# Performance work log

Measured on AMD Instinct MI355X. Metric: run time of the kernel, lower is better.

## Reference

```python
import jax, jax.numpy as jnp
import numpy as np

EPS = 1e-6
LN_EPS = 1e-6

def _mlstm_parallel_stabilized(q, k, v, igate_preact, fgate_preact):
    # q,k,v: (B,NH,S,DH); igate_preact,fgate_preact: (B,NH,S,1)
    B, NH, S, DH = q.shape
    log_fg = jax.nn.log_sigmoid(fgate_preact[..., 0])            # (B,NH,S)
    cs = jnp.cumsum(log_fg, axis=-1)                             # (B,NH,S)
    # log decay matrix: entry (i,j) = cumsum_i - cumsum_j, lower-triangular (j<=i)
    fg_mat = cs[..., :, None] - cs[..., None, :]                 # (B,NH,S,S)
    mask = jnp.tril(jnp.ones((S, S), dtype=bool))
    log_D = jnp.where(mask, fg_mat + igate_preact[..., 0][..., None, :], -jnp.inf)
    max_log_D = jnp.max(log_D, axis=-1, keepdims=True)           # (B,NH,S,1)
    D = jnp.exp(log_D - max_log_D)                               # (B,NH,S,S)
    k_scaled = k / jnp.sqrt(jnp.float32(DH)).astype(k.dtype)
    qk = jnp.einsum('bhsd,bhtd->bhst', q, k_scaled)              # (B,NH,S,S)
    C = qk * D
    normalizer = jnp.maximum(jnp.abs(jnp.sum(C, axis=-1, keepdims=True)), jnp.exp(-max_log_D))
    C_norm = C / (normalizer + EPS)
    return jnp.einsum('bhst,bhtd->bhsd', C_norm, v)              # (B,NH,S,DH)

def _multihead_layernorm(x, weight):
    # x: (B,NH,S,DH), weight: (NH,DH); normalize over DH per head, no bias
    mu = jnp.mean(x, axis=-1, keepdims=True)
    var = jnp.mean(jnp.square(x - mu), axis=-1, keepdims=True)
    xn = (x - mu) * jax.lax.rsqrt(var + LN_EPS)
    return xn * weight[None, :, None, :]

def setup_inputs() -> dict:
    key = jax.random.key(0)
    ks = jax.random.split(key, 6)
    B, S, E, NH = 2, 2048, 1024, 8
    q = jax.random.normal(ks[0], (B, S, E), dtype=jnp.float32)
    k = jax.random.normal(ks[1], (B, S, E), dtype=jnp.float32)
    v = jax.random.normal(ks[2], (B, S, E), dtype=jnp.float32)
    igate_kernel = jnp.zeros((3 * E, NH), dtype=jnp.float32)
    igate_bias = 0.1 * jax.random.normal(ks[3], (NH,), dtype=jnp.float32)
    fgate_kernel = jnp.zeros((3 * E, NH), dtype=jnp.float32)
    fgate_bias = jnp.linspace(3.0, 6.0, NH, dtype=jnp.float32)
    outnorm_weight = jnp.ones((NH, E // NH), dtype=jnp.float32)
    return {"q": q, "k": k, "v": v,
            "igate_kernel": igate_kernel, "igate_bias": igate_bias,
            "fgate_kernel": fgate_kernel, "fgate_bias": fgate_bias,
            "outnorm_weight": outnorm_weight}

def reference(q, k, v, igate_kernel, igate_bias, fgate_kernel, fgate_bias, outnorm_weight):
    B, S, E = q.shape
    NH = igate_bias.shape[0]
    qkv = jnp.concatenate([q, k, v], axis=-1)                    # (B,S,3E)
    igate_preact = qkv @ igate_kernel + igate_bias               # (B,S,NH)
    fgate_preact = qkv @ fgate_kernel + fgate_bias               # (B,S,NH)
    qh = q.reshape(B, S, NH, -1).transpose(0, 2, 1, 3)           # (B,NH,S,DH)
    kh = k.reshape(B, S, NH, -1).transpose(0, 2, 1, 3)
    vh = v.reshape(B, S, NH, -1).transpose(0, 2, 1, 3)
    ig = igate_preact.transpose(0, 2, 1)[..., None]              # (B,NH,S,1)
    fg = fgate_preact.transpose(0, 2, 1)[..., None]
    h = _mlstm_parallel_stabilized(qh, kh, vh, ig, fg)           # (B,NH,S,DH)
    h_norm = _multihead_layernorm(h, outnorm_weight)
    return h_norm.transpose(0, 2, 1, 3).reshape(B, S, -1)        # (B,S,E)
```

## Files before the change

### kernel.cpp

```cpp
#include <hip/hip_runtime.h>
#include <math.h>

#define S_LEN 2048
#define E_DIM 1024
#define NHEAD 8
#define DHEAD 128

typedef short bf16x8 __attribute__((ext_vector_type(8)));
typedef float f32x4 __attribute__((ext_vector_type(4)));
typedef unsigned int u32x4 __attribute__((ext_vector_type(4)));
typedef unsigned int u32x2 __attribute__((ext_vector_type(2)));

constexpr float RSQ_DH  = 0.08838834764831843f;
constexpr float LNRSQ   = -2.4260151319598084f;
constexpr float EPS_NORM = 1e-6f;
constexpr float LN_EPS_C = 1e-6f;

__device__ inline unsigned bfpair(float lo, float hi) {
  unsigned a = __builtin_bit_cast(unsigned, lo);
  unsigned b = __builtin_bit_cast(unsigned, hi);
  a = (a + 0x7fffu + ((a >> 16) & 1u)) >> 16;
  b = (b + 0x7fffu + ((b >> 16) & 1u)) >> 16;
  return a | (b << 16);
}

__device__ inline unsigned cvtpk(float lo, float hi) {
  unsigned r;
  asm("v_cvt_pk_bf16_f32 %0, %1, %2" : "=v"(r) : "v"(lo), "v"(hi));
  return r;
}

__device__ inline void gload_lds16(const void* g, void* lds) {
  __builtin_amdgcn_global_load_lds(
      (const __attribute__((address_space(1))) unsigned int*)g,
      (__attribute__((address_space(3))) unsigned int*)lds, 16, 0, 0);
}
__device__ inline void gload_lds4(const void* g, void* lds) {
  __builtin_amdgcn_global_load_lds(
      (const __attribute__((address_space(1))) unsigned int*)g,
      (__attribute__((address_space(3))) unsigned int*)lds, 4, 0, 0);
}

__global__ __launch_bounds__(256) void gates_fused(
    const float* __restrict__ q, const float* __restrict__ k, const float* __restrict__ v,
    const float* __restrict__ Wi, const float* __restrict__ bi,
    const float* __restrict__ Wf, const float* __restrict__ bf,
    float* __restrict__ ig_pre, float* __restrict__ fg_pre,
    unsigned short* __restrict__ kb) {
  const int t = threadIdx.x;
  const int row0 = blockIdx.x * 4;
  const int b = row0 >> 11;
  const int s0 = row0 & 2047;
  float p[4][16];
#pragma unroll
  for (int rr = 0; rr < 4; ++rr)
#pragma unroll
    for (int c = 0; c < 16; ++c) p[rr][c] = 0.f;

#pragma unroll
  for (int i = 0; i < 3; ++i) {
    const float* base = (i == 0) ? q : (i == 1) ? k : v;
    float xs[4][4];
#pragma unroll
    for (int rr = 0; rr < 4; ++rr) {
      const float4 xv = *(const float4*)(base + (size_t)(row0 + rr) * E_DIM + t * 4);
      xs[rr][0] = xv.x; xs[rr][1] = xv.y; xs[rr][2] = xv.z; xs[rr][3] = xv.w;
    }
#pragma unroll
    for (int j = 0; j < 4; ++j) {
      const int ge = i * E_DIM + t * 4 + j;
      const float4 wiA = *(const float4*)(Wi + (size_t)ge * 8);
      const float4 wiB = *(const float4*)(Wi + (size_t)ge * 8 + 4);
      const float4 wfA = *(const float4*)(Wf + (size_t)ge * 8);
      const float4 wfB = *(const float4*)(Wf + (size_t)ge * 8 + 4);
      const float wv16[16] = {wiA.x, wiA.y, wiA.z, wiA.w, wiB.x, wiB.y, wiB.z, wiB.w,
                              wfA.x, wfA.y, wfA.z, wfA.w, wfB.x, wfB.y, wfB.z, wfB.w};
#pragma unroll
      for (int rr = 0; rr < 4; ++rr) {
        const float x = xs[rr][j];
#pragma unroll
        for (int c = 0; c < 16; ++c) p[rr][c] += x * wv16[c];
      }
    }
    if (i == 1 && kb != nullptr) {
      const int h = (t * 4) >> 7, d = (t * 4) & 127;
#pragma unroll
      for (int rr = 0; rr < 4; ++rr) {
        u32x2 pk;
        pk.x = bfpair(xs[rr][0], xs[rr][1]);
        pk.y = bfpair(xs[rr][2], xs[rr][3]);
        *(u32x2*)(kb + (((size_t)b * NHEAD + h) * S_LEN + (s0 + rr)) * DHEAD + d) = pk;
      }
    }
  }

#pragma unroll
  for (int rr = 0; rr < 4; ++rr)
#pragma unroll
    for (int c = 0; c < 16; ++c) {
      float val = p[rr][c];
      val += __shfl_xor(val, 1);
      val += __shfl_xor(val, 2);
      val += __shfl_xor(val, 4);
      val += __shfl_xor(val, 8);
      val += __shfl_xor(val, 16);
      val += __shfl_xor(val, 32);
      p[rr][c] = val;
    }
  __shared__ float sred[4][4][16];
  const int wid = t >> 6, lane = t & 63;
  if (lane == 0) {
#pragma unroll
    for (int rr = 0; rr < 4; ++rr)
#pragma unroll
      for (int c = 0; c < 16; ++c) sred[wid][rr][c] = p[rr][c];
  }
  __syncthreads();
  if (t < 64) {
    const int rr = t >> 4, c = t & 15;
    float sum = sred[0][rr][c] + sred[1][rr][c] + sred[2][rr][c] + sred[3][rr][c];
    const int h = c & 7;
    const int row = row0 + rr;
    const int bb = row / S_LEN, s = row % S_LEN;
    if (c < 8) ig_pre[((size_t)bb * NHEAD + h) * S_LEN + s] = sum + bi[h];
    else       fg_pre[((size_t)bb * NHEAD + h) * S_LEN + s] = sum + bf[h];
  }
}

__global__ __launch_bounds__(256) void vtrans(const float* __restrict__ v,
                                              unsigned short* __restrict__ vtb) {
  __shared__ unsigned int tile[128][36];
  const int bid = blockIdx.x;
  const int bh = bid >> 5, st = bid & 31;
  const int b = bh >> 3, h = bh & 7;
  const int s0 = st * 64;
  const int t = threadIdx.x;
#pragma unroll
  for (int i = 0; i < 4; ++i) {
    const int task = t + 256 * i;
    const int sp = task & 31, dq = task >> 5;
    const float* src = v + ((size_t)b * S_LEN + s0 + 2 * sp) * E_DIM + h * DHEAD + dq * 4;
    const float4 r0 = *(const float4*)(src);
    const float4 r1 = *(const float4*)(src + E_DIM);
    tile[dq * 4 + 0][sp] = bfpair(r0.x, r1.x);
    tile[dq * 4 + 1][sp] = bfpair(r0.y, r1.y);
    tile[dq * 4 + 2][sp] = bfpair(r0.z, r1.z);
    tile[dq * 4 + 3][sp] = bfpair(r0.w, r1.w);
  }
  __syncthreads();
#pragma unroll
  for (int i = 0; i < 2; ++i) {
    const int task = t + 256 * i;
    const int d = task >> 2, c4 = task & 3;
    u32x4 w0, w1;
    w0.x = tile[d][c4 * 8 + 0]; w0.y = tile[d][c4 * 8 + 1];
    w0.z = tile[d][c4 * 8 + 2]; w0.w = tile[d][c4 * 8 + 3];
    w1.x = tile[d][c4 * 8 + 4]; w1.y = tile[d][c4 * 8 + 5];
    w1.z = tile[d][c4 * 8 + 6]; w1.w = tile[d][c4 * 8 + 7];
    unsigned short* dst = vtb + ((size_t)bh * DHEAD + d) * S_LEN + s0 + c4 * 16;
    *(u32x4*)(dst)     = w0;
    *(u32x4*)(dst + 8) = w1;
  }
}

__global__ __launch_bounds__(256) void scan_kernel(
    const float* __restrict__ ig_pre, const float* __restrict__ fg_pre,
    float* __restrict__ cs_out, float* __restrict__ g_out, float* __restrict__ gmax_out,
    float g_add) {
  const int bhh = blockIdx.x;
  const int t = threadIdx.x;
  const int lane = t & 63, wid = t >> 6;
  const size_t base = (size_t)bhh * S_LEN;
  float vals[8];
  float run = 0.f;
#pragma unroll
  for (int i = 0; i < 8; ++i) {
    const float x = fg_pre[base + t * 8 + i];
    const float lf = fminf(x, 0.f) - log1pf(__expf(-fabsf(x)));
    run += lf;
    vals[i] = run;
  }
  float ws = run;
#pragma unroll
  for (int off = 1; off < 64; off <<= 1) {
    const float v = __shfl_up(ws, off);
    if (lane >= off) ws += v;
  }
  __shared__ float wsum[4];
  if (lane == 63) wsum[wid] = ws;
  __syncthreads();
  float wpre = 0.f;
#pragma unroll
  for (int kk = 0; kk < 4; ++kk)
    if (kk < wid) wpre += wsum[kk];
  const float prefix = wpre + (ws - run);

  float g_loc[8], gm_loc[8];
  float lmax = -3.4e38f;
#pragma unroll
  for (int i = 0; i < 8; ++i) {
    const float csv = vals[i] + prefix;
    vals[i] = csv;
    const float gg = ig_pre[base + t * 8 + i] - csv;
    g_loc[i] = gg;
    lmax = fmaxf(lmax, gg);
    gm_loc[i] = lmax;
  }
  float wm = lmax;
#pragma unroll
  for (int off = 1; off < 64; off <<= 1) {
    const float v = __shfl_up(wm, off);
    if (lane >= off) wm = fmaxf(wm, v);
  }
  __shared__ float wmax[4];
  if (lane == 63) wmax[wid] = wm;
  __syncthreads();
  float mpre = -3.4e38f;
#pragma unroll
  for (int kk = 0; kk < 4; ++kk)
    if (kk < wid) mpre = fmaxf(mpre, wmax[kk]);
  float excl = __shfl_up(wm, 1);
  if (lane == 0) excl = -3.4e38f;
  const float pmax = fmaxf(mpre, excl);

#pragma unroll
  for (int i = 0; i < 8; ++i) {
    cs_out[base + t * 8 + i]   = vals[i];
    g_out[base + t * 8 + i]    = g_loc[i] + g_add;
    gmax_out[base + t * 8 + i] = fmaxf(gm_loc[i], pmax);
  }
}

__global__ __launch_bounds__(256) void mlstm_mfma9(
    const unsigned short* __restrict__ kb, const unsigned short* __restrict__ vtb,
    const float* __restrict__ q,
    const float* __restrict__ cs, const float* __restrict__ garr, const float* __restrict__ gmax,
    const float* __restrict__ wgt, float* __restrict__ out) {
  __shared__ __align__(16) unsigned char kbuf[4][8192];
  __shared__ __align__(16) unsigned char vbuf[4][8192];
  __shared__ float g_sh[4][32];
  __shared__ float den_sh[4][64];

  const int bid = blockIdx.x;
  int qb;
  if (bid < 256) qb = 31 - (bid >> 4);
  else           qb = (bid - 256) >> 4;
  const int g16 = bid & 15;
  const int bh = 2 * (g16 & 7) + (g16 >> 3);
  const int b = bh >> 3, h = bh & 7;
  const int t = threadIdx.x;
  const int w = t >> 6;
  const int iw = w & 1;
  const int tp = w >> 1;
  const int l = t & 63;
  const int r = l & 15;
  const int qq = l >> 4;
  const size_t bhS = (size_t)bh * S_LEN;

  const int grA = qb * 64 + 4 * r + 2 * iw;
  const int grB = grA + 1;
  const float gmA = gmax[bhS + grA];
  const float gmB = gmax[bhS + grB];
  const float rAB = __expf(gmA - gmB);

  bf16x8 qfA[4], qfB[4];
  {
    const float* qrowA = q + ((size_t)b * S_LEN + grA) * E_DIM + h * DHEAD;
    const float* qrowB = q + ((size_t)b * S_LEN + grB) * E_DIM + h * DHEAD;
#pragma unroll
    for (int c = 0; c < 4; ++c) {
      float4 f0 = *(const float4*)(qrowA + 32 * c + 8 * qq);
      float4 f1 = *(const float4*)(qrowA + 32 * c + 8 * qq + 4);
      u32x4 u;
      u.x = bfpair(f0.x, f0.y); u.y = bfpair(f0.z, f0.w);
      u.z = bfpair(f1.x, f1.y); u.w = bfpair(f1.z, f1.w);
      qfA[c] = __builtin_bit_cast(bf16x8, u);
      f0 = *(const float4*)(qrowB + 32 * c + 8 * qq);
      f1 = *(const float4*)(qrowB + 32 * c + 8 * qq + 4);
      u.x = bfpair(f0.x, f0.y); u.y = bfpair(f0.z, f0.w);
      u.z = bfpair(f1.x, f1.y); u.w = bfpair(f1.z, f1.w);
      qfB[c] = __builtin_bit_cast(bf16x8, u);
    }
  }

  f32x4 oA[8], oB[8];
#pragma unroll
  for (int n = 0; n < 8; ++n) { oA[n] = (f32x4){0,0,0,0}; oB[n] = (f32x4){0,0,0,0}; }
  float denA = 0.f, denB = 0.f;

  const unsigned short* kt = kb + bhS * DHEAD;
  const unsigned short* vt = vtb + (size_t)bh * DHEAD * S_LEN;

  auto stage = [&](int pair, int set) {
    const int j0 = pair * 64 + tp * 32;
    const int bi = set * 2 + tp;
#pragma unroll
    for (int a = 0; a < 4; ++a) {
      const int m = iw * 256 + a * 64 + l;
      const int u = m ^ ((m >> 4) & 7);
      gload_lds16(kt + ((size_t)(j0 + (u >> 4))) * DHEAD + (u & 15) * 8,
                  &kbuf[bi][(iw * 256 + a * 64) * 16]);
    }
#pragma unroll
    for (int a = 0; a < 4; ++a) {
      const int m = iw * 256 + a * 64 + l;
      const int u = m ^ ((m >> 3) & 7);
      gload_lds16(vt + (size_t)(u >> 2) * S_LEN + j0 + (u & 3) * 8,
                  &vbuf[bi][(iw * 256 + a * 64) * 16]);
    }
    if (l < 32) gload_lds4(garr + bhS + j0 + l, &g_sh[bi][0]);
  };

  auto body = [&](int j0, int bi, bool diag) {
    __builtin_amdgcn_s_setprio(1);
    f32x4 sA0 = {0,0,0,0}, sA1 = {0,0,0,0}, sB0 = {0,0,0,0}, sB1 = {0,0,0,0};
#pragma unroll
    for (int c = 0; c < 4; ++c) {
      const int u0 = ((r)      * 16 + 4 * c + qq) ^ (r & 7);
      const int u1 = ((16 + r) * 16 + 4 * c + qq) ^ (r & 7);
      bf16x8 ka0 = *(const bf16x8*)&kbuf[bi][u0 * 16];
      bf16x8 ka1 = *(const bf16x8*)&kbuf[bi][u1 * 16];
      sA0 = __builtin_amdgcn_mfma_f32_16x16x32_bf16(ka0, qfA[c], sA0, 0, 0, 0);
      sB0 = __builtin_amdgcn_mfma_f32_16x16x32_bf16(ka0, qfB[c], sB0, 0, 0, 0);
      sA1 = __builtin_amdgcn_mfma_f32_16x16x32_bf16(ka1, qfA[c], sA1, 0, 0, 0);
      sB1 = __builtin_amdgcn_mfma_f32_16x16x32_bf16(ka1, qfB[c], sB1, 0, 0, 0);
    }
    __builtin_amdgcn_s_setprio(0);

    unsigned PA0[2], PA1[2], PB0[2], PB1[2];
    {
      float wa[4], wb[4];
#pragma unroll
      for (int m = 0; m < 4; ++m) {
        const int jl = 4 * qq + m;
        const float e = __expf(g_sh[bi][jl] - gmA);
        float a = sA0[m] * e;
        float bq = sB0[m] * e * rAB;
        if (diag) {
          if (j0 + jl > grA) a = 0.f;
          if (j0 + jl > grB) bq = 0.f;
        }
        wa[m] = a; wb[m] = bq; denA += a; denB += bq;
      }
      PA0[0] = cvtpk(wa[0], wa[1]); PA0[1] = cvtpk(wa[2], wa[3]);
      PB0[0] = cvtpk(wb[0], wb[1]); PB0[1] = cvtpk(wb[2], wb[3]);
#pragma unroll
      for (int m = 0; m < 4; ++m) {
        const int jl = 16 + 4 * qq + m;
        const float e = __expf(g_sh[bi][jl] - gmA);
        float a = sA1[m] * e;
        float bq = sB1[m] * e * rAB;
        if (diag) {
          if (j0 + jl > grA) a = 0.f;
          if (j0 + jl > grB) bq = 0.f;
        }
        wa[m] = a; wb[m] = bq; denA += a; denB += bq;
      }
      PA1[0] = cvtpk(wa[0], wa[1]); PA1[1] = cvtpk(wa[2], wa[3]);
      PB1[0] = cvtpk(wb[0], wb[1]); PB1[1] = cvtpk(wb[2], wb[3]);
    }

    unsigned AA[4], AB[4];
#pragma unroll
    for (int m = 0; m < 4; ++m) {
      const int srcl = r + 16 * (2 * (qq & 1) + (m >> 1));
      const unsigned a0 = (unsigned)__shfl((int)PA0[m & 1], srcl);
      const unsigned a1 = (unsigned)__shfl((int)PA1[m & 1], srcl);
      const unsigned b0 = (unsigned)__shfl((int)PB0[m & 1], srcl);
      const unsigned b1 = (unsigned)__shfl((int)PB1[m & 1], srcl);
      AA[m] = (qq < 2) ? a0 : a1;
      AB[m] = (qq < 2) ? b0 : b1;
    }
    u32x4 ua, ub;
    ua.x = AA[0]; ua.y = AA[1]; ua.z = AA[2]; ua.w = AA[3];
    ub.x = AB[0]; ub.y = AB[1]; ub.z = AB[2]; ub.w = AB[3];
    const bf16x8 paA = __builtin_bit_cast(bf16x8, ua);
    const bf16x8 paB = __builtin_bit_cast(bf16x8, ub);

    __builtin_amdgcn_s_setprio(1);
#pragma unroll
    for (int n = 0; n < 8; ++n) {
      const int ud = (16 * n + r) * 4 + qq;
      const int up = ud ^ ((ud >> 3) & 7);
      bf16x8 vb = *(const bf16x8*)&vbuf[bi][up * 16];
      oA[n] = __builtin_amdgcn_mfma_f32_16x16x32_bf16(paA, vb, oA[n], 0, 0, 0);
      oB[n] = __builtin_amdgcn_mfma_f32_16x16x32_bf16(paB, vb, oB[n], 0, 0, 0);
    }
    __builtin_amdgcn_s_setprio(0);
  };

  stage(0, 0);
  for (int p = 0; p < qb; ++p) {
    stage(p + 1, (p + 1) & 1);
    asm volatile("s_waitcnt vmcnt(9)" ::: "memory");
    __builtin_amdgcn_sched_barrier(0);
    __syncthreads();
    body(p * 64 + tp * 32, (p & 1) * 2 + tp, false);
    __syncthreads();
  }
  asm volatile("s_waitcnt vmcnt(0)" ::: "memory");
  __builtin_amdgcn_sched_barrier(0);
  __syncthreads();
  body(qb * 64 + tp * 32, (qb & 1) * 2 + tp, true);

  float* osh = (float*)&kbuf[0][0];
  __syncthreads();
  const int xsw = (r & 7) << 2;
  if (tp == 1) {
#pragma unroll
    for (int n = 0; n < 8; ++n) {
      const int i0 = ((((16 * n + r) * 2 + iw) * 2 + 0) * 16 + 4 * qq) ^ xsw;
      const int i1 = ((((16 * n + r) * 2 + iw) * 2 + 1) * 16 + 4 * qq) ^ xsw;
      *(f32x4*)&osh[i0] = oA[n];
      *(f32x4*)&osh[i1] = oB[n];
    }
    den_sh[iw * 2 + 0][l] = denA;
    den_sh[iw * 2 + 1][l] = denB;
  }
  __syncthreads();
  if (tp == 0) {
    denA += den_sh[iw * 2 + 0][l];
    denB += den_sh[iw * 2 + 1][l];
#pragma unroll
    for (int n = 0; n < 8; ++n) {
      const int i0 = ((((16 * n + r) * 2 + iw) * 2 + 0) * 16 + 4 * qq) ^ xsw;
      const int i1 = ((((16 * n + r) * 2 + iw) * 2 + 1) * 16 + 4 * qq) ^ xsw;
      oA[n] += *(const f32x4*)&osh[i0];
      oB[n] += *(const f32x4*)&osh[i1];
    }

    const float* wrow = wgt + h * DHEAD;
    float wv_n[8];
#pragma unroll
    for (int n = 0; n < 8; ++n) wv_n[n] = wrow[16 * n + r];

#pragma unroll
    for (int fg = 0; fg < 2; ++fg) {
      float den_f = (fg == 0) ? denA : denB;
      den_f += __shfl_xor(den_f, 16);
      den_f += __shfl_xor(den_f, 32);
#pragma unroll
      for (int m = 0; m < 4; ++m) {
        const int iloc = 4 * qq + m;
        const float den_o = __shfl(den_f, iloc);
        const int grow = qb * 64 + 4 * iloc + 2 * iw + fg;
        const float csg = cs[bhS + grow];
        const float gmg = gmax[bhS + grow];
        const float norm = fmaxf(fabsf(den_o), __expf(-(csg + gmg))) + EPS_NORM;
        const float inv = 1.f / norm;
        float hv[8];
        float s1 = 0.f, s2 = 0.f;
#pragma unroll
        for (int n = 0; n < 8; ++n) {
          hv[n] = ((fg == 0) ? oA[n][m] : oB[n][m]) * inv;
          s1 += hv[n]; s2 += hv[n] * hv[n];
        }
        s1 += __shfl_xor(s1, 1); s1 += __shfl_xor(s1, 2);
        s1 += __shfl_xor(s1, 4); s1 += __shfl_xor(s1, 8);
        s2 += __shfl_xor(s2, 1); s2 += __shfl_xor(s2, 2);
        s2 += __shfl_xor(s2, 4); s2 += __shfl_xor(s2, 8);
        const float mu  = s1 * (1.f / 128.f);
        const float var = s2 * (1.f / 128.f) - mu * mu;
        const float rstd = rsqrtf(var + LN_EPS_C);
        float* orow = out + ((size_t)b * S_LEN + grow) * E_DIM + h * DHEAD;
#pragma unroll
        for (int n = 0; n < 8; ++n)
          orow[16 * n + r] = (hv[n] - mu) * rstd * wv_n[n];
      }
    }
  }
}

__global__ __launch_bounds__(256) void mlstm_mfma(
    const float* __restrict__ q, const float* __restrict__ k, const float* __restrict__ v,
    const float* __restrict__ cs, const float* __restrict__ garr, const float* __restrict__ gmax,
    const float* __restrict__ wgt, float* __restrict__ out) {
  __shared__ unsigned short k_lds[32][136];
  __shared__ unsigned int   vt_u32[128][20];
  __shared__ unsigned int   xch[4][16][20];
  __shared__ float          g_sh[32];

  const int bid = blockIdx.x;
  int qt;
  if (bid < 256) qt = 31 - (bid >> 4);
  else           qt = (bid - 256) >> 4;
  const int bh = bid & 15;
  const int b = bh >> 3, h = bh & 7;
  const int t = threadIdx.x;
  const int w = t >> 6;
  const int l = t & 63;
  const int r = l & 15;
  const int qq = l >> 4;
  const size_t bhS = (size_t)bh * S_LEN;

  const int gr = qt * 64 + 4 * r + w;
  const float gm_lane = gmax[bhS + gr];

  bf16x8 qfrag[4];
  {
    const float* qrow = q + ((size_t)b * S_LEN + gr) * E_DIM + h * DHEAD;
#pragma unroll
    for (int c = 0; c < 4; ++c) {
      const float4 f0 = *(const float4*)(qrow + 32 * c + 8 * qq);
      const float4 f1 = *(const float4*)(qrow + 32 * c + 8 * qq + 4);
      u32x4 u;
      u.x = bfpair(f0.x, f0.y); u.y = bfpair(f0.z, f0.w);
      u.z = bfpair(f1.x, f1.y); u.w = bfpair(f1.z, f1.w);
      qfrag[c] = __builtin_bit_cast(bf16x8, u);
    }
  }

  f32x4 o[8];
#pragma unroll
  for (int n = 0; n < 8; ++n) o[n] = (f32x4){0.f, 0.f, 0.f, 0.f};
  float den_p = 0.f;

  const int kj = t >> 3, ks = t & 7;
  const int vjp = t & 15, vds = t >> 4;

  const int ntiles = 2 * qt + 2;
  for (int jt = 0; jt < ntiles; ++jt) {
    const int j0 = jt * 32;
    {
      const float* src = k + ((size_t)b * S_LEN + j0 + kj) * E_DIM + h * DHEAD + ks * 16;
      float4 f0 = *(const float4*)(src);
      float4 f1 = *(const float4*)(src + 4);
      float4 f2 = *(const float4*)(src + 8);
      float4 f3 = *(const float4*)(src + 12);
      u32x4 ua, ub;
      ua.x = bfpair(f0.x, f0.y); ua.y = bfpair(f0.z, f0.w);
      ua.z = bfpair(f1.x, f1.y); ua.w = bfpair(f1.z, f1.w);
      ub.x = bfpair(f2.x, f2.y); ub.y = bfpair(f2.z, f2.w);
      ub.z = bfpair(f3.x, f3.y); ub.w = bfpair(f3.z, f3.w);
      *(u32x4*)&k_lds[kj][ks * 16]     = ua;
      *(u32x4*)&k_lds[kj][ks * 16 + 8] = ub;
    }
    {
      const float* s0 = v + ((size_t)b * S_LEN + j0 + 2 * vjp) * E_DIM + h * DHEAD + vds * 8;
      const float* s1 = s0 + E_DIM;
      float4 a0 = *(const float4*)(s0);
      float4 a1 = *(const float4*)(s0 + 4);
      float4 b0 = *(const float4*)(s1);
      float4 b1 = *(const float4*)(s1 + 4);
      vt_u32[vds * 8 + 0][vjp] = bfpair(a0.x, b0.x);
      vt_u32[vds * 8 + 1][vjp] = bfpair(a0.y, b0.y);
      vt_u32[vds * 8 + 2][vjp] = bfpair(a0.z, b0.z);
      vt_u32[vds * 8 + 3][vjp] = bfpair(a0.w, b0.w);
      vt_u32[vds * 8 + 4][vjp] = bfpair(a1.x, b1.x);
      vt_u32[vds * 8 + 5][vjp] = bfpair(a1.y, b1.y);
      vt_u32[vds * 8 + 6][vjp] = bfpair(a1.z, b1.z);
      vt_u32[vds * 8 + 7][vjp] = bfpair(a1.w, b1.w);
    }
    if (t < 32) g_sh[t] = garr[bhS + j0 + t];
    __syncthreads();

    f32x4 st0 = {0, 0, 0, 0}, st1 = {0, 0, 0, 0};
#pragma unroll
    for (int c = 0; c < 4; ++c) {
      bf16x8 ka0 = *(const bf16x8*)&k_lds[r][32 * c + 8 * qq];
      bf16x8 ka1 = *(const bf16x8*)&k_lds[16 + r][32 * c + 8 * qq];
      st0 = __builtin_amdgcn_mfma_f32_16x16x32_bf16(ka0, qfrag[c], st0, 0, 0, 0);
      st1 = __builtin_amdgcn_mfma_f32_16x16x32_bf16(ka1, qfrag[c], st1, 0, 0, 0);
    }

    const bool diag = (jt >= 2 * qt);
    float wv0[4], wv1[4];
#pragma unroll
    for (int reg = 0; reg < 4; ++reg) {
      const int jl0 = 4 * qq + reg, jl1 = 16 + 4 * qq + reg;
      const float e0 = __expf(g_sh[jl0] - gm_lane);
      const float e1 = __expf(g_sh[jl1] - gm_lane);
      float w0 = st0[reg] * RSQ_DH * e0;
      float w1 = st1[reg] * RSQ_DH * e1;
      if (diag) {
        if (j0 + jl0 > gr) w0 = 0.f;
        if (j0 + jl1 > gr) w1 = 0.f;
      }
      wv0[reg] = w0; wv1[reg] = w1;
      den_p += w0 + w1;
    }

    u32x2 p0, p1;
    p0.x = bfpair(wv0[0], wv0[1]); p0.y = bfpair(wv0[2], wv0[3]);
    p1.x = bfpair(wv1[0], wv1[1]); p1.y = bfpair(wv1[2], wv1[3]);
    *(u32x2*)&xch[w][r][2 * qq]     = p0;
    *(u32x2*)&xch[w][r][8 + 2 * qq] = p1;
    __builtin_amdgcn_wave_barrier();
    bf16x8 pa = *(const bf16x8*)&xch[w][r][4 * qq];
    __builtin_amdgcn_wave_barrier();

#pragma unroll
    for (int n = 0; n < 8; ++n) {
      bf16x8 vb = *(const bf16x8*)&vt_u32[16 * n + r][4 * qq];
      o[n] = __builtin_amdgcn_mfma_f32_16x16x32_bf16(pa, vb, o[n], 0, 0, 0);
    }
    __syncthreads();
  }

  float den_f = den_p;
  den_f += __shfl_xor(den_f, 16);
  den_f += __shfl_xor(den_f, 32);

  const float* wrow = wgt + h * DHEAD;
  float wv_n[8];
#pragma unroll
  for (int n = 0; n < 8; ++n) wv_n[n] = wrow[16 * n + r];

#pragma unroll
  for (int reg = 0; reg < 4; ++reg) {
    const int iloc = 4 * qq + reg;
    const float den_o = __shfl(den_f, iloc);
    const int grow = qt * 64 + 4 * iloc + w;
    const float csg = cs[bhS + grow];
    const float gmg = gmax[bhS + grow];
    const float norm = fmaxf(fabsf(den_o), __expf(-(csg + gmg))) + EPS_NORM;
    const float inv = 1.f / norm;
    float hv[8];
    float s1 = 0.f, s2 = 0.f;
#pragma unroll
    for (int n = 0; n < 8; ++n) {
      hv[n] = o[n][reg] * inv;
      s1 += hv[n]; s2 += hv[n] * hv[n];
    }
    s1 += __shfl_xor(s1, 1); s1 += __shfl_xor(s1, 2);
    s1 += __shfl_xor(s1, 4); s1 += __shfl_xor(s1, 8);
    s2 += __shfl_xor(s2, 1); s2 += __shfl_xor(s2, 2);
    s2 += __shfl_xor(s2, 4); s2 += __shfl_xor(s2, 8);
    const float mu  = s1 * (1.f / 128.f);
    const float var = s2 * (1.f / 128.f) - mu * mu;
    const float rstd = rsqrtf(var + LN_EPS_C);
    float* orow = out + ((size_t)b * S_LEN + grow) * E_DIM + h * DHEAD;
#pragma unroll
    for (int n = 0; n < 8; ++n)
      orow[16 * n + r] = (hv[n] - mu) * rstd * wv_n[n];
  }
}

extern "C" void kernel_launch(void* const* d_in, const int* in_sizes, int n_in,
                              void* d_out, int out_size, void* d_ws, size_t ws_size,
                              hipStream_t stream) {
  (void)in_sizes; (void)n_in; (void)out_size;
  const float* q   = (const float*)d_in[0];
  const float* k   = (const float*)d_in[1];
  const float* v   = (const float*)d_in[2];
  const float* Wi  = (const float*)d_in[3];
  const float* bi  = (const float*)d_in[4];
  const float* Wf  = (const float*)d_in[5];
  const float* bf  = (const float*)d_in[6];
  const float* wgt = (const float*)d_in[7];
  float* out = (float*)d_out;
  float* ws  = (float*)d_ws;
  const int BNS = 2 * NHEAD * S_LEN;
  float* ig_pre = ws;
  float* fg_pre = ws + (size_t)BNS;
  float* cs     = ws + (size_t)2 * BNS;
  float* gv     = ws + (size_t)3 * BNS;
  float* gmaxs  = ws + (size_t)4 * BNS;
  unsigned short* kb  = (unsigned short*)(ws + (size_t)5 * BNS);
  unsigned short* vtb = kb + (size_t)16 * S_LEN * DHEAD;

  const size_t need = (size_t)5 * BNS * 4 + (size_t)2 * 16 * S_LEN * DHEAD * 2;

  if (ws_size >= need) {
    gates_fused<<<1024, 256, 0, stream>>>(q, k, v, Wi, bi, Wf, bf, ig_pre, fg_pre, kb);
    vtrans<<<512, 256, 0, stream>>>(v, vtb);
    scan_kernel<<<16, 256, 0, stream>>>(ig_pre, fg_pre, cs, gv, gmaxs, LNRSQ);
    mlstm_mfma9<<<512, 256, 0, stream>>>(kb, vtb, q, cs, gv, gmaxs, wgt, out);
  } else {
    gates_fused<<<1024, 256, 0, stream>>>(q, k, v, Wi, bi, Wf, bf, ig_pre, fg_pre, nullptr);
    scan_kernel<<<16, 256, 0, stream>>>(ig_pre, fg_pre, cs, gv, gmaxs, 0.0f);
    mlstm_mfma<<<512, 256, 0, stream>>>(q, k, v, cs, gv, gmaxs, wgt, out);
  }
}
```

Before: 102.1 us.

## Split long causal query blocks across two workgroups with flag-based partial-sum merge

Adds a persistent-style kernel in which the 16 longest query blocks per head are split into two halves along the key dimension. The first half writes partial outputs and denominators to workspace and raises a flag; the second half spin-waits on that flag, merges the partials, and applies normalization and layernorm. Remaining short blocks are taken from an atomic work counter. The aim is to balance the triangular causal workload across CUs and shorten the tail. The cost is extra workspace traffic, a memset, and a spin-wait that relies on both halves being resident at the same time. The old fp32 fallback kernel is removed, and mlstm_mfma9 becomes the fallback.

```diff
diff --git a/kernel.cpp b/kernel.cpp
--- a/kernel.cpp
+++ b/kernel.cpp
@@ -228,6 +228,314 @@
     cs_out[base + t * 8 + i]   = vals[i];
     g_out[base + t * 8 + i]    = g_loc[i] + g_add;
     gmax_out[base + t * 8 + i] = fmaxf(gm_loc[i], pmax);
+  }
+}
+
+__global__ __launch_bounds__(256) void mlstm_qd(
+    const unsigned short* __restrict__ kb, const unsigned short* __restrict__ vtb,
+    const float* __restrict__ q,
+    const float* __restrict__ cs, const float* __restrict__ garr, const float* __restrict__ gmax,
+    const float* __restrict__ wgt, float* __restrict__ out,
+    int* __restrict__ flags, int* __restrict__ qctr,
+    float* __restrict__ po, float* __restrict__ pden) {
+  __shared__ __align__(16) unsigned char kbuf[4][8192];
+  __shared__ __align__(16) unsigned char vbuf[4][8192];
+  __shared__ float g_sh[4][32];
+  __shared__ float den_sh[4][64];
+  __shared__ int item_sh;
+
+  const int t = threadIdx.x;
+  const int w = t >> 6;
+  const int iw = w & 1;
+  const int tp = w >> 1;
+  const int l = t & 63;
+  const int r = l & 15;
+  const int qq = l >> 4;
+
+  int item = blockIdx.x;
+  while (item < 768) {
+    int qb, jp0, npair, g16, nparts, slot = 0, half = 0;
+    if (item < 512) {
+      qb = 31 - (item >> 5);
+      half = (item >> 4) & 1;
+      g16 = item & 15;
+      const int P = qb + 1, h0 = P >> 1;
+      jp0 = half ? h0 : 0;
+      npair = half ? (P - h0) : h0;
+      nparts = 2;
+      slot = (qb - 16) * 16 + g16;
+    } else {
+      qb = 15 - ((item - 512) >> 4);
+      g16 = item & 15;
+      jp0 = 0; npair = qb + 1; nparts = 1;
+    }
+    const int bh = 2 * (g16 & 7) + (g16 >> 3);
+    const int b = bh >> 3, h = bh & 7;
+    const size_t bhS = (size_t)bh * S_LEN;
+
+    const int grA = qb * 64 + 4 * r + 2 * iw;
+    const int grB = grA + 1;
+    const float gmA = gmax[bhS + grA];
+    const float gmB = gmax[bhS + grB];
+    const float rAB = __expf(gmA - gmB);
+
+    bf16x8 qfA[4], qfB[4];
+    {
+      const float* qrowA = q + ((size_t)b * S_LEN + grA) * E_DIM + h * DHEAD;
+      const float* qrowB = q + ((size_t)b * S_LEN + grB) * E_DIM + h * DHEAD;
+#pragma unroll
+      for (int c = 0; c < 4; ++c) {
+        float4 f0 = *(const float4*)(qrowA + 32 * c + 8 * qq);
+        float4 f1 = *(const float4*)(qrowA + 32 * c + 8 * qq + 4);
+        u32x4 u;
+        u.x = bfpair(f0.x, f0.y); u.y = bfpair(f0.z, f0.w);
+        u.z = bfpair(f1.x, f1.y); u.w = bfpair(f1.z, f1.w);
+        qfA[c] = __builtin_bit_cast(bf16x8, u);
+        f0 = *(const float4*)(qrowB + 32 * c + 8 * qq);
+        f1 = *(const float4*)(qrowB + 32 * c + 8 * qq + 4);
+        u.x = bfpair(f0.x, f0.y); u.y = bfpair(f0.z, f0.w);
+        u.z = bfpair(f1.x, f1.y); u.w = bfpair(f1.z, f1.w);
+        qfB[c] = __builtin_bit_cast(bf16x8, u);
+      }
+    }
+
+    f32x4 oA[8], oB[8];
+#pragma unroll
+    for (int n = 0; n < 8; ++n) { oA[n] = (f32x4){0,0,0,0}; oB[n] = (f32x4){0,0,0,0}; }
+    float denA = 0.f, denB = 0.f;
+
+    const unsigned short* kt = kb + bhS * DHEAD;
+    const unsigned short* vt = vtb + (size_t)bh * DHEAD * S_LEN;
+
+    auto stage = [&](int pair, int set) {
+      const int j0 = pair * 64 + tp * 32;
+      const int bi = set * 2 + tp;
+#pragma unroll
+      for (int a = 0; a < 4; ++a) {
+        const int m = iw * 256 + a * 64 + l;
+        const int u = m ^ ((m >> 4) & 7);
+        gload_lds16(kt + ((size_t)(j0 + (u >> 4))) * DHEAD + (u & 15) * 8,
+                    &kbuf[bi][(iw * 256 + a * 64) * 16]);
+      }
+#pragma unroll
+      for (int a = 0; a < 4; ++a) {
+        const int m = iw * 256 + a * 64 + l;
+        const int u = m ^ ((m >> 3) & 7);
+        gload_lds16(vt + (size_t)(u >> 2) * S_LEN + j0 + (u & 3) * 8,
+                    &vbuf[bi][(iw * 256 + a * 64) * 16]);
+      }
+      if (l < 32) gload_lds4(garr + bhS + j0 + l, &g_sh[bi][0]);
+    };
+
+    auto body = [&](int j0, int bi, bool diag) {
+      __builtin_amdgcn_s_setprio(1);
+      f32x4 sA0 = {0,0,0,0}, sA1 = {0,0,0,0}, sB0 = {0,0,0,0}, sB1 = {0,0,0,0};
+#pragma unroll
+      for (int c = 0; c < 4; ++c) {
+        const int u0 = ((r)      * 16 + 4 * c + qq) ^ (r & 7);
+        const int u1 = ((16 + r) * 16 + 4 * c + qq) ^ (r & 7);
+        bf16x8 ka0 = *(const bf16x8*)&kbuf[bi][u0 * 16];
+        bf16x8 ka1 = *(const bf16x8*)&kbuf[bi][u1 * 16];
+        sA0 = __builtin_amdgcn_mfma_f32_16x16x32_bf16(ka0, qfA[c], sA0, 0, 0, 0);
+        sB0 = __builtin_amdgcn_mfma_f32_16x16x32_bf16(ka0, qfB[c], sB0, 0, 0, 0);
+        sA1 = __builtin_amdgcn_mfma_f32_16x16x32_bf16(ka1, qfA[c], sA1, 0, 0, 0);
+        sB1 = __builtin_amdgcn_mfma_f32_16x16x32_bf16(ka1, qfB[c], sB1, 0, 0, 0);
+      }
+      __builtin_amdgcn_s_setprio(0);
+
+      unsigned PA0[2], PA1[2], PB0[2], PB1[2];
+      {
+        float wa[4], wb[4];
+#pragma unroll
+        for (int m = 0; m < 4; ++m) {
+          const int jl = 4 * qq + m;
+          const float e = __expf(g_sh[bi][jl] - gmA);
+          float a = sA0[m] * e;
+          float bq = sB0[m] * e * rAB;
+          if (diag) {
+            if (j0 + jl > grA) a = 0.f;
+            if (j0 + jl > grB) bq = 0.f;
+          }
+          wa[m] = a; wb[m] = bq; denA += a; denB += bq;
+        }
+        PA0[0] = cvtpk(wa[0], wa[1]); PA0[1] = cvtpk(wa[2], wa[3]);
+        PB0[0] = cvtpk(wb[0], wb[1]); PB0[1] = cvtpk(wb[2], wb[3]);
+#pragma unroll
+        for (int m = 0; m < 4; ++m) {
+          const int jl = 16 + 4 * qq + m;
+          const float e = __expf(g_sh[bi][jl] - gmA);
+          float a = sA1[m] * e;
+          float bq = sB1[m] * e * rAB;
+          if (diag) {
+            if (j0 + jl > grA) a = 0.f;
+            if (j0 + jl > grB) bq = 0.f;
+          }
+          wa[m] = a; wb[m] = bq; denA += a; denB += bq;
+        }
+        PA1[0] = cvtpk(wa[0], wa[1]); PA1[1] = cvtpk(wa[2], wa[3]);
+        PB1[0] = cvtpk(wb[0], wb[1]); PB1[1] = cvtpk(wb[2], wb[3]);
+      }
+
+      unsigned AA[4], AB[4];
+#pragma unroll
+      for (int m = 0; m < 4; ++m) {
+        const int srcl = r + 16 * (2 * (qq & 1) + (m >> 1));
+        const unsigned a0 = (unsigned)__shfl((int)PA0[m & 1], srcl);
+        const unsigned a1 = (unsigned)__shfl((int)PA1[m & 1], srcl);
+        const unsigned b0 = (unsigned)__shfl((int)PB0[m & 1], srcl);
+        const unsigned b1 = (unsigned)__shfl((int)PB1[m & 1], srcl);
+        AA[m] = (qq < 2) ? a0 : a1;
+        AB[m] = (qq < 2) ? b0 : b1;
+      }
+      u32x4 ua, ub;
+      ua.x = AA[0]; ua.y = AA[1]; ua.z = AA[2]; ua.w = AA[3];
+      ub.x = AB[0]; ub.y = AB[1]; ub.z = AB[2]; ub.w = AB[3];
+      const bf16x8 paA = __builtin_bit_cast(bf16x8, ua);
+      const bf16x8 paB = __builtin_bit_cast(bf16x8, ub);
+
+      __builtin_amdgcn_s_setprio(1);
+#pragma unroll
+      for (int n = 0; n < 8; ++n) {
+        const int ud = (16 * n + r) * 4 + qq;
+        const int up = ud ^ ((ud >> 3) & 7);
+        bf16x8 vb = *(const bf16x8*)&vbuf[bi][up * 16];
+        oA[n] = __builtin_amdgcn_mfma_f32_16x16x32_bf16(paA, vb, oA[n], 0, 0, 0);
+        oB[n] = __builtin_amdgcn_mfma_f32_16x16x32_bf16(paB, vb, oB[n], 0, 0, 0);
+      }
+      __builtin_amdgcn_s_setprio(0);
+    };
+
+    stage(jp0, 0);
+    for (int pi = 0; pi + 1 < npair; ++pi) {
+      stage(jp0 + pi + 1, (pi + 1) & 1);
+      asm volatile("s_waitcnt vmcnt(9)" ::: "memory");
+      __builtin_amdgcn_sched_barrier(0);
+      __syncthreads();
+      body((jp0 + pi) * 64 + tp * 32, (pi & 1) * 2 + tp, false);
+      __syncthreads();
+    }
+    asm volatile("s_waitcnt vmcnt(0)" ::: "memory");
+    __builtin_amdgcn_sched_barrier(0);
+    __syncthreads();
+    {
+      const int pi = npair - 1;
+      const bool dg = (jp0 + pi) == qb;
+      body((jp0 + pi) * 64 + tp * 32, (pi & 1) * 2 + tp, dg);
+    }
+
+    float* osh = (float*)&kbuf[0][0];
+    __syncthreads();
+    const int xsw = (r & 7) << 2;
+    if (tp == 1) {
+#pragma unroll
+      for (int n = 0; n < 8; ++n) {
+        const int i0 = ((((16 * n + r) * 2 + iw) * 2 + 0) * 16 + 4 * qq) ^ xsw;
+        const int i1 = ((((16 * n + r) * 2 + iw) * 2 + 1) * 16 + 4 * qq) ^ xsw;
+        *(f32x4*)&osh[i0] = oA[n];
+        *(f32x4*)&osh[i1] = oB[n];
+      }
+      den_sh[iw * 2 + 0][l] = denA;
+      den_sh[iw * 2 + 1][l] = denB;
+    }
+    __syncthreads();
+    if (tp == 0) {
+      denA += den_sh[iw * 2 + 0][l];
+      denB += den_sh[iw * 2 + 1][l];
+#pragma unroll
+      for (int n = 0; n < 8; ++n) {
+        const int i0 = ((((16 * n + r) * 2 + iw) * 2 + 0) * 16 + 4 * qq) ^ xsw;
+        const int i1 = ((((16 * n + r) * 2 + iw) * 2 + 1) * 16 + 4 * qq) ^ xsw;
+        oA[n] += *(const f32x4*)&osh[i0];
+        oB[n] += *(const f32x4*)&osh[i1];
+      }
+    }
+    __syncthreads();
+
+    bool do_ln = false;
+    if (nparts == 2 && half == 0) {
+      if (tp == 0) {
+        float* ps = po + (size_t)slot * 8192;
+#pragma unroll
+        for (int n = 0; n < 8; ++n) {
+          const int i0 = (((16 * n + r) * 2 + iw) * 2 + 0) * 16 + 4 * qq;
+          const int i1 = (((16 * n + r) * 2 + iw) * 2 + 1) * 16 + 4 * qq;
+          *(f32x4*)&ps[i0] = oA[n];
+          *(f32x4*)&ps[i1] = oB[n];
+        }
+        pden[slot * 256 + (iw * 2 + 0) * 64 + l] = denA;
+        pden[slot * 256 + (iw * 2 + 1) * 64 + l] = denB;
+      }
+      __threadfence();
+      __syncthreads();
+      if (t == 0) atomicExch(&flags[slot], 1);
+    } else if (nparts == 2) {
+      if (t == 0) {
+        while (atomicAdd(&flags[slot], 0) == 0) __builtin_amdgcn_s_sleep(16);
+      }
+      __syncthreads();
+      __threadfence();
+      if (tp == 0) {
+        const float* ps = po + (size_t)slot * 8192;
+#pragma unroll
+        for (int n = 0; n < 8; ++n) {
+          const int i0 = (((16 * n + r) * 2 + iw) * 2 + 0) * 16 + 4 * qq;
+          const int i1 = (((16 * n + r) * 2 + iw) * 2 + 1) * 16 + 4 * qq;
+          oA[n] += *(const f32x4*)&ps[i0];
+          oB[n] += *(const f32x4*)&ps[i1];
+        }
+        denA += pden[slot * 256 + (iw * 2 + 0) * 64 + l];
+        denB += pden[slot * 256 + (iw * 2 + 1) * 64 + l];
+      }
+      do_ln = true;
+    } else {
+      do_ln = true;
+    }
+
+    if (do_ln && tp == 0) {
+      const float* wrow = wgt + h * DHEAD;
+      float wv_n[8];
+#pragma unroll
+      for (int n = 0; n < 8; ++n) wv_n[n] = wrow[16 * n + r];
+#pragma unroll
+      for (int fg = 0; fg < 2; ++fg) {
+        float den_f = (fg == 0) ? denA : denB;
+        den_f += __shfl_xor(den_f, 16);
+        den_f += __shfl_xor(den_f, 32);
+#pragma unroll
+        for (int m = 0; m < 4; ++m) {
+          const int iloc = 4 * qq + m;
+          const float den_o = __shfl(den_f, iloc);
+          const int grow = qb * 64 + 4 * iloc + 2 * iw + fg;
+          const float csg = cs[bhS + grow];
+          const float gmg = gmax[bhS + grow];
+          const float norm = fmaxf(fabsf(den_o), __expf(-(csg + gmg))) + EPS_NORM;
+          const float inv = 1.f / norm;
+          float hv[8];
+          float s1 = 0.f, s2 = 0.f;
+#pragma unroll
+          for (int n = 0; n < 8; ++n) {
+            hv[n] = ((fg == 0) ? oA[n][m] : oB[n][m]) * inv;
+            s1 += hv[n]; s2 += hv[n] * hv[n];
+          }
+          s1 += __shfl_xor(s1, 1); s1 += __shfl_xor(s1, 2);
+          s1 += __shfl_xor(s1, 4); s1 += __shfl_xor(s1, 8);
+          s2 += __shfl_xor(s2, 1); s2 += __shfl_xor(s2, 2);
+          s2 += __shfl_xor(s2, 4); s2 += __shfl_xor(s2, 8);
+          const float mu  = s1 * (1.f / 128.f);
+          const float var = s2 * (1.f / 128.f) - mu * mu;
+          const float rstd = rsqrtf(var + LN_EPS_C);
+          float* orow = out + ((size_t)b * S_LEN + grow) * E_DIM + h * DHEAD;
+#pragma unroll
+          for (int n = 0; n < 8; ++n)
+            orow[16 * n + r] = (hv[n] - mu) * rstd * wv_n[n];
+        }
+      }
+    }
+
+    __syncthreads();
+    if (t == 0) item_sh = 512 + atomicAdd(qctr, 1);
+    __syncthreads();
+    item = item_sh;
   }
 }
 
@@ -468,171 +776,6 @@
           orow[16 * n + r] = (hv[n] - mu) * rstd * wv_n[n];
       }
     }
-  }
-}
-
-__global__ __launch_bounds__(256) void mlstm_mfma(
-    const float* __restrict__ q, const float* __restrict__ k, const float* __restrict__ v,
-    const float* __restrict__ cs, const float* __restrict__ garr, const float* __restrict__ gmax,
-    const float* __restrict__ wgt, float* __restrict__ out) {
-  __shared__ unsigned short k_lds[32][136];
-  __shared__ unsigned int   vt_u32[128][20];
-  __shared__ unsigned int   xch[4][16][20];
-  __shared__ float          g_sh[32];
-
-  const int bid = blockIdx.x;
-  int qt;
-  if (bid < 256) qt = 31 - (bid >> 4);
-  else           qt = (bid - 256) >> 4;
-  const int bh = bid & 15;
-  const int b = bh >> 3, h = bh & 7;
-  const int t = threadIdx.x;
-  const int w = t >> 6;
-  const int l = t & 63;
-  const int r = l & 15;
-  const int qq = l >> 4;
-  const size_t bhS = (size_t)bh * S_LEN;
-
-  const int gr = qt * 64 + 4 * r + w;
-  const float gm_lane = gmax[bhS + gr];
-
-  bf16x8 qfrag[4];
-  {
-    const float* qrow = q + ((size_t)b * S_LEN + gr) * E_DIM + h * DHEAD;
-#pragma unroll
-    for (int c = 0; c < 4; ++c) {
-      const float4 f0 = *(const float4*)(qrow + 32 * c + 8 * qq);
-      const float4 f1 = *(const float4*)(qrow + 32 * c + 8 * qq + 4);
-      u32x4 u;
-      u.x = bfpair(f0.x, f0.y); u.y = bfpair(f0.z, f0.w);
-      u.z = bfpair(f1.x, f1.y); u.w = bfpair(f1.z, f1.w);
-      qfrag[c] = __builtin_bit_cast(bf16x8, u);
-    }
-  }
-
-  f32x4 o[8];
-#pragma unroll
-  for (int n = 0; n < 8; ++n) o[n] = (f32x4){0.f, 0.f, 0.f, 0.f};
-  float den_p = 0.f;
-
-  const int kj = t >> 3, ks = t & 7;
-  const int vjp = t & 15, vds = t >> 4;
-
-  const int ntiles = 2 * qt + 2;
-  for (int jt = 0; jt < ntiles; ++jt) {
-    const int j0 = jt * 32;
-    {
-      const float* src = k + ((size_t)b * S_LEN + j0 + kj) * E_DIM + h * DHEAD + ks * 16;
-      float4 f0 = *(const float4*)(src);
-      float4 f1 = *(const float4*)(src + 4);
-      float4 f2 = *(const float4*)(src + 8);
-      float4 f3 = *(const float4*)(src + 12);
-      u32x4 ua, ub;
-      ua.x = bfpair(f0.x, f0.y); ua.y = bfpair(f0.z, f0.w);
-      ua.z = bfpair(f1.x, f1.y); ua.w = bfpair(f1.z, f1.w);
-      ub.x = bfpair(f2.x, f2.y); ub.y = bfpair(f2.z, f2.w);
-      ub.z = bfpair(f3.x, f3.y); ub.w = bfpair(f3.z, f3.w);
-      *(u32x4*)&k_lds[kj][ks * 16]     = ua;
-      *(u32x4*)&k_lds[kj][ks * 16 + 8] = ub;
-    }
-    {
-      const float* s0 = v + ((size_t)b * S_LEN + j0 + 2 * vjp) * E_DIM + h * DHEAD + vds * 8;
-      const float* s1 = s0 + E_DIM;
-      float4 a0 = *(const float4*)(s0);
-      float4 a1 = *(const float4*)(s0 + 4);
-      float4 b0 = *(const float4*)(s1);
-      float4 b1 = *(const float4*)(s1 + 4);
-      vt_u32[vds * 8 + 0][vjp] = bfpair(a0.x, b0.x);
-      vt_u32[vds * 8 + 1][vjp] = bfpair(a0.y, b0.y);
-      vt_u32[vds * 8 + 2][vjp] = bfpair(a0.z, b0.z);
-      vt_u32[vds * 8 + 3][vjp] = bfpair(a0.w, b0.w);
-      vt_u32[vds * 8 + 4][vjp] = bfpair(a1.x, b1.x);
-      vt_u32[vds * 8 + 5][vjp] = bfpair(a1.y, b1.y);
-      vt_u32[vds * 8 + 6][vjp] = bfpair(a1.z, b1.z);
-      vt_u32[vds * 8 + 7][vjp] = bfpair(a1.w, b1.w);
-    }
-    if (t < 32) g_sh[t] = garr[bhS + j0 + t];
-    __syncthreads();
-
-    f32x4 st0 = {0, 0, 0, 0}, st1 = {0, 0, 0, 0};
-#pragma unroll
-    for (int c = 0; c < 4; ++c) {
-      bf16x8 ka0 = *(const bf16x8*)&k_lds[r][32 * c + 8 * qq];
-      bf16x8 ka1 = *(const bf16x8*)&k_lds[16 + r][32 * c + 8 * qq];
-      st0 = __builtin_amdgcn_mfma_f32_16x16x32_bf16(ka0, qfrag[c], st0, 0, 0, 0);
-      st1 = __builtin_amdgcn_mfma_f32_16x16x32_bf16(ka1, qfrag[c], st1, 0, 0, 0);
-    }
-
-    const bool diag = (jt >= 2 * qt);
-    float wv0[4], wv1[4];
-#pragma unroll
-    for (int reg = 0; reg < 4; ++reg) {
-      const int jl0 = 4 * qq + reg, jl1 = 16 + 4 * qq + reg;
-      const float e0 = __expf(g_sh[jl0] - gm_lane);
-      const float e1 = __expf(g_sh[jl1] - gm_lane);
-      float w0 = st0[reg] * RSQ_DH * e0;
-      float w1 = st1[reg] * RSQ_DH * e1;
-      if (diag) {
-        if (j0 + jl0 > gr) w0 = 0.f;
-        if (j0 + jl1 > gr) w1 = 0.f;
-      }
-      wv0[reg] = w0; wv1[reg] = w1;
-      den_p += w0 + w1;
-    }
-
-    u32x2 p0, p1;
-    p0.x = bfpair(wv0[0], wv0[1]); p0.y = bfpair(wv0[2], wv0[3]);
-    p1.x = bfpair(wv1[0], wv1[1]); p1.y = bfpair(wv1[2], wv1[3]);
-    *(u32x2*)&xch[w][r][2 * qq]     = p0;
-    *(u32x2*)&xch[w][r][8 + 2 * qq] = p1;
-    __builtin_amdgcn_wave_barrier();
-    bf16x8 pa = *(const bf16x8*)&xch[w][r][4 * qq];
-    __builtin_amdgcn_wave_barrier();
-
-#pragma unroll
-    for (int n = 0; n < 8; ++n) {
-      bf16x8 vb = *(const bf16x8*)&vt_u32[16 * n + r][4 * qq];
-      o[n] = __builtin_amdgcn_mfma_f32_16x16x32_bf16(pa, vb, o[n], 0, 0, 0);
-    }
-    __syncthreads();
-  }
-
-  float den_f = den_p;
-  den_f += __shfl_xor(den_f, 16);
-  den_f += __shfl_xor(den_f, 32);
-
-  const float* wrow = wgt + h * DHEAD;
-  float wv_n[8];
-#pragma unroll
-  for (int n = 0; n < 8; ++n) wv_n[n] = wrow[16 * n + r];
-
-#pragma unroll
-  for (int reg = 0; reg < 4; ++reg) {
-    const int iloc = 4 * qq + reg;
-    const float den_o = __shfl(den_f, iloc);
-    const int grow = qt * 64 + 4 * iloc + w;
-    const float csg = cs[bhS + grow];
-    const float gmg = gmax[bhS + grow];
-    const float norm = fmaxf(fabsf(den_o), __expf(-(csg + gmg))) + EPS_NORM;
-    const float inv = 1.f / norm;
-    float hv[8];
-    float s1 = 0.f, s2 = 0.f;
-#pragma unroll
-    for (int n = 0; n < 8; ++n) {
-      hv[n] = o[n][reg] * inv;
-      s1 += hv[n]; s2 += hv[n] * hv[n];
-    }
-    s1 += __shfl_xor(s1, 1); s1 += __shfl_xor(s1, 2);
-    s1 += __shfl_xor(s1, 4); s1 += __shfl_xor(s1, 8);
-    s2 += __shfl_xor(s2, 1); s2 += __shfl_xor(s2, 2);
-    s2 += __shfl_xor(s2, 4); s2 += __shfl_xor(s2, 8);
-    const float mu  = s1 * (1.f / 128.f);
-    const float var = s2 * (1.f / 128.f) - mu * mu;
-    const float rstd = rsqrtf(var + LN_EPS_C);
-    float* orow = out + ((size_t)b * S_LEN + grow) * E_DIM + h * DHEAD;
-#pragma unroll
-    for (int n = 0; n < 8; ++n)
-      orow[16 * n + r] = (hv[n] - mu) * rstd * wv_n[n];
   }
 }
 
@@ -658,17 +801,25 @@
   float* gmaxs  = ws + (size_t)4 * BNS;
   unsigned short* kb  = (unsigned short*)(ws + (size_t)5 * BNS);
   unsigned short* vtb = kb + (size_t)16 * S_LEN * DHEAD;
-
-  const size_t need = (size_t)5 * BNS * 4 + (size_t)2 * 16 * S_LEN * DHEAD * 2;
-
-  if (ws_size >= need) {
+  float* po   = (float*)(vtb + (size_t)16 * S_LEN * DHEAD);
+  float* pden = po + (size_t)256 * 8192;
+  int*   flags = (int*)(pden + (size_t)256 * 256);
+  int*   qctr  = flags + 256;
+
+  const size_t need9 = (size_t)5 * BNS * 4 + (size_t)2 * 16 * S_LEN * DHEAD * 2;
+  const size_t needQ = need9 + ((size_t)256 * 8192 + 256 * 256) * 4 + 257 * 4;
+
+  if (ws_size >= needQ) {
+    hipMemsetAsync(flags, 0, 257 * 4, stream);
+    gates_fused<<<1024, 256, 0, stream>>>(q, k, v, Wi, bi, Wf, bf, ig_pre, fg_pre, kb);
+    vtrans<<<512, 256, 0, stream>>>(v, vtb);
+    scan_kernel<<<16, 256, 0, stream>>>(ig_pre, fg_pre, cs, gv, gmaxs, LNRSQ);
+    mlstm_qd<<<512, 256, 0, stream>>>(kb, vtb, q, cs, gv, gmaxs, wgt, out,
+                                      flags, qctr, po, pden);
+  } else {
     gates_fused<<<1024, 256, 0, stream>>>(q, k, v, Wi, bi, Wf, bf, ig_pre, fg_pre, kb);
     vtrans<<<512, 256, 0, stream>>>(v, vtb);
     scan_kernel<<<16, 256, 0, stream>>>(ig_pre, fg_pre, cs, gv, gmaxs, LNRSQ);
     mlstm_mfma9<<<512, 256, 0, stream>>>(kb, vtb, q, cs, gv, gmaxs, wgt, out);
-  } else {
-    gates_fused<<<1024, 256, 0, stream>>>(q, k, v, Wi, bi, Wf, bf, ig_pre, fg_pre, nullptr);
-    scan_kernel<<<16, 256, 0, stream>>>(ig_pre, fg_pre, cs, gv, gmaxs, 0.0f);
-    mlstm_mfma<<<512, 256, 0, stream>>>(q, k, v, cs, gv, gmaxs, wgt, out);
-  }
-}
+  }
+}
```

Result: slower. 184.5 us (+80.7%).
